# Kernel optimization log

Measured on AMD Instinct MI355X. Metric: run time of the kernel, lower is better.

Reference implementation:

```python
import jax, jax.numpy as jnp
import numpy as np

N = 20000          # num proposals (nodes)
E = 320000         # num edges
IN = 4096          # roi feature dim
EMB = 200          # glove embed dim
HID = 512          # hidden dim
NH = 8             # heads (conv1)
HC = HID // NH     # 64 per-head channels
NCLS = 151         # VG object classes
NEG_SLOPE = 0.2    # PyG GATConv leaky_relu slope


def setup_inputs() -> dict:
    key = jax.random.key(0)
    ks = jax.random.split(key, 18)
    d_in1 = IN + EMB + 128  # 4424, conv1 input dim
    inp = {
        "roi_features": jax.random.normal(ks[0], (N, IN), jnp.float32),
        "box_info": jax.random.uniform(ks[1], (N, 9), jnp.float32),
        # embedding tables
        "emb1": jax.random.normal(ks[2], (NCLS, EMB), jnp.float32) * 0.02,
        "emb2": jax.random.normal(ks[3], (NCLS, EMB), jnp.float32) * 0.02,
        # bbox MLP 9 -> 32 -> 128
        "bw1": jax.random.normal(ks[4], (9, 32), jnp.float32) / np.sqrt(9),
        "bb1": jnp.zeros((32,), jnp.float32),
        "bw2": jax.random.normal(ks[5], (32, 128), jnp.float32) / np.sqrt(32),
        "bb2": jnp.zeros((128,), jnp.float32),
        # GATConv1: d_in1 -> 8 heads x 64, concat
        "W1": jax.random.normal(ks[6], (d_in1, NH * HC), jnp.float32) / np.sqrt(d_in1),
        "a_src1": jax.random.normal(ks[7], (NH, HC), jnp.float32) * 0.1,
        "a_dst1": jax.random.normal(ks[8], (NH, HC), jnp.float32) * 0.1,
        "bias1": jnp.zeros((NH * HC,), jnp.float32),
        # GATConv2: 512 -> 512, 1 head, concat=False
        "W2": jax.random.normal(ks[9], (HID, HID), jnp.float32) / np.sqrt(HID),
        "a_src2": jax.random.normal(ks[10], (1, HID), jnp.float32) * 0.1,
        "a_dst2": jax.random.normal(ks[11], (1, HID), jnp.float32) * 0.1,
        "bias2": jnp.zeros((HID,), jnp.float32),
        # int inputs
        "obj_labels": jax.random.randint(ks[12], (N,), 0, NCLS, jnp.int32),
        "edge_index": jax.random.randint(ks[13], (2, E), 0, N, jnp.int32),
    }
    return inp


def _segment_softmax(logits, seg, n):
    # logits: [E, H]; softmax over edges sharing the same destination seg id
    m = jax.ops.segment_max(logits, seg, num_segments=n)
    e = jnp.exp(logits - m[seg])
    s = jax.ops.segment_sum(e, seg, num_segments=n)
    return e / (s[seg] + 1e-16)


def _gat_conv(x, src, dst, W, a_src, a_dst, bias, concat):
    # PyG GATConv (self-loops already included in src/dst); dropout off (eval)
    n = x.shape[0]
    H, C = a_src.shape
    h = (x @ W).reshape(n, H, C)                      # [N, H, C]
    al_s = jnp.einsum('nhc,hc->nh', h, a_src)         # [N, H]
    al_d = jnp.einsum('nhc,hc->nh', h, a_dst)
    logits = jax.nn.leaky_relu(al_s[src] + al_d[dst], NEG_SLOPE)  # [E, H]
    alpha = _segment_softmax(logits, dst, n)          # [E, H]
    out = jax.ops.segment_sum(alpha[:, :, None] * h[src], dst, num_segments=n)
    out = out.reshape(n, H * C) if concat else out.mean(axis=1)
    return out + bias


def reference(roi_features, box_info, emb1, emb2, bw1, bb1, bw2, bb2,
              W1, a_src1, a_dst1, bias1, W2, a_src2, a_dst2, bias2,
              obj_labels, edge_index):
    n = roi_features.shape[0]
    # predcls mode: GT labels -> embedding lookup
    obj_embed = emb1[obj_labels]                              # [N, 200]
    pos = jax.nn.relu(box_info @ bw1 + bb1)
    pos = jax.nn.relu(pos @ bw2 + bb2)                        # [N, 128]
    x = jnp.concatenate([roi_features, obj_embed, pos], -1)  # [N, 4424]

    # add self-loops (PyG GATConv default)
    ar = jnp.arange(n, dtype=edge_index.dtype)
    src = jnp.concatenate([edge_index[0], ar])
    dst = jnp.concatenate([edge_index[1], ar])

    edge_f1 = jax.nn.elu(_gat_conv(x, src, dst, W1, a_src1, a_dst1, bias1, True))
    obj_feats = _gat_conv(edge_f1, src, dst, W2, a_src2, a_dst2, bias2, False)

    obj_dists = jax.nn.one_hot(obj_labels, NCLS, dtype=jnp.float32)
    edge_pre_rep = jnp.concatenate([roi_features, obj_feats, emb2[obj_labels]], -1)
    return obj_dists, obj_labels, edge_pre_rep
```

## Files before the change

### kernel.cpp

```cpp
#include <hip/hip_runtime.h>
#include <hip/hip_bf16.h>

#define NNODES 20000
#define NEDGES 320000
#define ETOT   (NEDGES + NNODES)
#define KPADX  4224
#define MPAD   20096
#define NCLS   151
#define EPRW   4808
#define OUT_LAB_OFF  3020000L
#define OUT_EPR_OFF  3040000L
#define NSLOPE 0.2f

typedef __attribute__((ext_vector_type(8))) short bf16x8;
typedef __attribute__((ext_vector_type(4))) float f32x4;
typedef __attribute__((ext_vector_type(4))) short s16x4;

__device__ __forceinline__ short f2bf(float v) {
  union { __hip_bfloat16 b; short s; } u;
  u.b = __float2bfloat16(v);
  return u.s;
}

__device__ __forceinline__ float bf2f(short s) {
  union { float f; unsigned u; } x;
  x.u = ((unsigned)(unsigned short)s) << 16;
  return x.f;
}

__device__ __forceinline__ void gld16(const short* g, short* l) {
  __builtin_amdgcn_global_load_lds(
      (const __attribute__((address_space(1))) unsigned int*)g,
      (__attribute__((address_space(3))) unsigned int*)l, 16, 0, 0);
}

#define PB0 20000
#define PB1 (PB0 + 1584)
#define PB2 (PB1 + 2112)
#define PB3 (PB2 + 256)
#define PB4 (PB3 + 1329)
#define PB5 (PB4 + 151)

__global__ __launch_bounds__(256) void mega_prep_kernel(
    const float* __restrict__ roi, const float* __restrict__ box,
    const float* __restrict__ emb1, const float* __restrict__ emb2,
    const float* __restrict__ bw1, const float* __restrict__ bb1,
    const float* __restrict__ bw2, const float* __restrict__ bb2,
    const float* __restrict__ W1, const float* __restrict__ W2,
    const int* __restrict__ labels, const int* __restrict__ ei,
    short* __restrict__ x, short* __restrict__ w1t, short* __restrict__ w2t,
    short* __restrict__ ef1, int* __restrict__ deg,
    float* __restrict__ als1, float* __restrict__ ald1,
    float* __restrict__ als2, float* __restrict__ ald2,
    float* __restrict__ E1, float* __restrict__ dout) {
  const int b = blockIdx.x;
  const int tid = threadIdx.x;

  __shared__ float hid[32];
  __shared__ float bx[9];
  __shared__ float tile[32][33];

  if (b < PB0) {
    const int n = b;
    if (tid < 9) bx[tid] = box[n * 9 + tid];
    __syncthreads();
    if (tid < 32) {
      float a = bb1[tid];
#pragma unroll
      for (int i = 0; i < 9; ++i) a += bx[i] * bw1[i * 32 + tid];
      hid[tid] = a > 0.f ? a : 0.f;
    }
    __syncthreads();
    const long xrow = (long)n * KPADX;
    if (tid < 128) {
      float a = bb2[tid];
#pragma unroll
      for (int i = 0; i < 32; ++i) a += hid[i] * bw2[i * 128 + tid];
      a = a > 0.f ? a : 0.f;
      x[xrow + 4096 + tid] = f2bf(a);
    }
    const int lab = labels[n];
    float* epr = dout + OUT_EPR_OFF + (long)n * EPRW;
#pragma unroll
    for (int j = tid * 4; j < 4096; j += 1024) {
      const f32x4 v = *(const f32x4*)&roi[(long)n * 4096 + j];
      __builtin_nontemporal_store(v, (f32x4*)&epr[j]);
      s16x4 bb;
      bb.x = f2bf(v.x); bb.y = f2bf(v.y); bb.z = f2bf(v.z); bb.w = f2bf(v.w);
      *(s16x4*)&x[xrow + j] = bb;
    }
    if (tid < 50) {
      const int j = tid * 4;
      const f32x4 e2 = *(const f32x4*)&emb2[lab * 200 + j];
      __builtin_nontemporal_store(e2, (f32x4*)&epr[4608 + j]);
    }
    for (int j = tid; j < NCLS; j += 256)
      dout[(long)n * NCLS + j] = (j == lab) ? 1.f : 0.f;
    if (tid == 0) dout[OUT_LAB_OFF + n] = (float)lab;
  } else if (b < PB1) {
    const int t = (b - PB0) * 256 + tid;
    if (t < 96 * KPADX) x[(long)NNODES * KPADX + t] = 0;
    if (t < 96 * 512)   ef1[(long)NNODES * 512 + t] = 0;
    if (t < MPAD * 8)   { als1[t] = 0.f; ald1[t] = 0.f; }
    if (t < MPAD)       { als2[t] = 0.f; ald2[t] = 0.f; }
  } else if (b < PB2) {
    const int t = b - PB1;
    const int n0 = (t % 16) * 32;
    const int k0 = (t / 16) * 32;
    const int tx = tid & 31, ty = tid >> 5;
#pragma unroll
    for (int i = ty; i < 32; i += 8) {
      const int kp = k0 + i;
      const int src = kp < 4096 ? kp : kp + 200;
      tile[i][tx] = W1[(long)src * 512 + (n0 + tx)];
    }
    __syncthreads();
#pragma unroll
    for (int i = ty; i < 32; i += 8)
      w1t[(long)(n0 + i) * KPADX + (k0 + tx)] = f2bf(tile[tx][i]);
  } else if (b < PB3) {
    const int t = b - PB2;
    const int n0 = (t % 16) * 32;
    const int k0 = (t / 16) * 32;
    const int tx = tid & 31, ty = tid >> 5;
#pragma unroll
    for (int i = ty; i < 32; i += 8)
      tile[i][tx] = W2[(long)(k0 + i) * 512 + (n0 + tx)];
    __syncthreads();
#pragma unroll
    for (int i = ty; i < 32; i += 8)
      w2t[(long)(n0 + i) * 512 + (k0 + tx)] = f2bf(tile[tx][i]);
  } else if (b < PB4) {
    const int e = (b - PB3) * 256 + tid;
    if (e < ETOT) {
      const int d = (e < NEDGES) ? ei[NEDGES + e] : (e - NEDGES);
      atomicAdd(&deg[d], 1);
    }
  } else {
    const int c = b - PB4;
#pragma unroll
    for (int jj = 0; jj < 2; ++jj) {
      const int j = tid + jj * 256;
      float a = 0.f;
      for (int k = 0; k < 200; ++k)
        a += emb1[c * 200 + k] * W1[(long)(4096 + k) * 512 + j];
      E1[c * 512 + j] = a;
    }
  }
}

__global__ __launch_bounds__(256) void scan_kernel(const int* __restrict__ deg,
                                                   int* __restrict__ off,
                                                   int* __restrict__ cur) {
  __shared__ int part[256];
  const int tid = threadIdx.x;
  const int chunk = (NNODES + 255) / 256;
  int start = tid * chunk;
  int end = start + chunk; if (end > NNODES) end = NNODES;
  int s = 0;
  for (int i = start; i < end; ++i) s += deg[i];
  part[tid] = s;
  __syncthreads();
  for (int d = 1; d < 256; d <<= 1) {
    const int v = (tid >= d) ? part[tid - d] : 0;
    __syncthreads();
    part[tid] += v;
    __syncthreads();
  }
  int base = part[tid] - s;
  for (int i = start; i < end; ++i) { off[i] = base; cur[i] = base; base += deg[i]; }
}

__global__ void csr_fill_kernel(const int* __restrict__ ei, int* __restrict__ cur,
                                int* __restrict__ csrs) {
  const int e = blockIdx.x * 256 + threadIdx.x;
  if (e >= ETOT) return;
  const int s = (e < NEDGES) ? ei[e] : (e - NEDGES);
  const int d = (e < NEDGES) ? ei[NEDGES + e] : (e - NEDGES);
  unsigned slot = (unsigned)atomicAdd(&cur[d], 1);
  if (slot >= ETOT) slot = 0;
  csrs[slot] = s;
}

__global__ __launch_bounds__(256) void gemm_bt(const short* __restrict__ A,
                                               const short* __restrict__ BT,
                                               short* __restrict__ C,
                                               const float* __restrict__ aS,
                                               const float* __restrict__ aD,
                                               float* __restrict__ als,
                                               float* __restrict__ ald,
                                               const float* __restrict__ E1,
                                               const int* __restrict__ labels,
                                               int Kpad, int Ncols, int H) {
  __shared__ short As[4096];
  __shared__ short Bs[4096];
  const int tid = threadIdx.x;
  const int lane = tid & 63;
  const int w = tid >> 6;
  const int wr = w >> 1, wc = w & 1;
  const int nbn = Ncols >> 7;
  const long bm = (long)((int)blockIdx.x / nbn) * 128;
  const long bn = (long)((int)blockIdx.x % nbn) * 128;

  f32x4 acc[4][4] = {};

  const short* gA0 = A + (bm + w * 32 + (lane >> 2)) * (long)Kpad + (lane & 3) * 8;
  const short* gA1 = gA0 + 16L * Kpad;
  const short* gB0 = BT + (bn + w * 32 + (lane >> 2)) * (long)Kpad + (lane & 3) * 8;
  const short* gB1 = gB0 + 16L * Kpad;
  short* lA0 = &As[w * 1024];
  short* lA1 = &As[w * 1024 + 512];
  short* lB0 = &Bs[w * 1024];
  short* lB1 = &Bs[w * 1024 + 512];

  const int ar = (wr * 64 + (lane & 15)) * 32 + (lane >> 4) * 8;
  const int br = (wc * 64 + (lane & 15)) * 32 + (lane >> 4) * 8;

  for (int k0 = 0; k0 < Kpad; k0 += 32) {
    gld16(gA0, lA0); gld16(gA1, lA1);
    gld16(gB0, lB0); gld16(gB1, lB1);
    gA0 += 32; gA1 += 32; gB0 += 32; gB1 += 32;
    asm volatile("s_waitcnt vmcnt(0)" ::: "memory");
    __syncthreads();
    bf16x8 a[4], b[4];
#pragma unroll
    for (int mi = 0; mi < 4; ++mi) a[mi] = *(const bf16x8*)&As[ar + mi * 512];
#pragma unroll
    for (int ni = 0; ni < 4; ++ni) b[ni] = *(const bf16x8*)&Bs[br + ni * 512];
#pragma unroll
    for (int mi = 0; mi < 4; ++mi)
#pragma unroll
      for (int ni = 0; ni < 4; ++ni)
        acc[mi][ni] = __builtin_amdgcn_mfma_f32_16x16x32_bf16(a[mi], b[ni], acc[mi][ni], 0, 0, 0);
    __syncthreads();
  }

  const int colb = (int)bn + wc * 64 + (lane & 15);

  if (E1) {
#pragma unroll
    for (int mi = 0; mi < 4; ++mi) {
#pragma unroll
      for (int r = 0; r < 4; ++r) {
        const long row = bm + wr * 64 + mi * 16 + (lane >> 4) * 4 + r;
        const int lb = (row < NNODES) ? labels[row] : 0;
        const float* e1r = E1 + (long)lb * 512;
#pragma unroll
        for (int ni = 0; ni < 4; ++ni)
          acc[mi][ni][r] += e1r[colb + ni * 16];
      }
    }
  }

#pragma unroll
  for (int mi = 0; mi < 4; ++mi) {
#pragma unroll
    for (int ni = 0; ni < 4; ++ni) {
      const long row0 = bm + wr * 64 + mi * 16 + (lane >> 4) * 4;
      const long col  = bn + wc * 64 + ni * 16 + (lane & 15);
#pragma unroll
      for (int r = 0; r < 4; ++r)
        C[(row0 + r) * (long)Ncols + col] = f2bf(acc[mi][ni][r]);
    }
  }

  float asv[4], adv[4];
#pragma unroll
  for (int ni = 0; ni < 4; ++ni) {
    asv[ni] = aS[colb + ni * 16];
    adv[ni] = aD[colb + ni * 16];
  }
  const int head = (H == 8) ? (((int)bn >> 6) + wc) : 0;
#pragma unroll
  for (int mi = 0; mi < 4; ++mi) {
#pragma unroll
    for (int r = 0; r < 4; ++r) {
      float s = 0.f, d = 0.f;
#pragma unroll
      for (int ni = 0; ni < 4; ++ni) {
        const float v = acc[mi][ni][r];
        s += v * asv[ni];
        d += v * adv[ni];
      }
#pragma unroll
      for (int o = 1; o < 16; o <<= 1) {
        s += __shfl_xor(s, o);
        d += __shfl_xor(d, o);
      }
      if ((lane & 15) == 0) {
        const long row = bm + wr * 64 + mi * 16 + (lane >> 4) * 4 + r;
        atomicAdd(&als[row * H + head], s);
        atomicAdd(&ald[row * H + head], d);
      }
    }
  }
}

__global__ __launch_bounds__(256) void gather1_kernel(const int* __restrict__ off,
    const int* __restrict__ csrs,
    const float* __restrict__ als, const float* __restrict__ ald,
    const short* __restrict__ h1, const float* __restrict__ bias,
    short* __restrict__ ef1) {
  const int dn = blockIdx.x * 4 + (threadIdx.x >> 6);
  const int lane = threadIdx.x & 63;
  const int c0 = lane * 8;
  const int head = lane >> 3;
  const int beg = off[dn];
  const int end = (dn == NNODES - 1) ? ETOT : off[dn + 1];
  const float ad = ald[dn * 8 + head];
  float sum = 0.f;
  float acc[8] = {};
  for (int i = beg; i < end; ++i) {
    int s = csrs[i];
    if ((unsigned)s >= NNODES) s = 0;
    float l = als[s * 8 + head] + ad;
    l = l > 0.f ? l : NSLOPE * l;
    const float wgt = expf(l);
    sum += wgt;
    const bf16x8 hv = *(const bf16x8*)&h1[(long)s * 512 + c0];
#pragma unroll
    for (int j = 0; j < 8; ++j) acc[j] += wgt * bf2f(hv[j]);
  }
  const float inv = 1.f / (sum + 1e-16f);
  bf16x8 outv;
#pragma unroll
  for (int j = 0; j < 8; ++j) {
    float r = acc[j] * inv + bias[c0 + j];
    r = r > 0.f ? r : expm1f(r);
    outv[j] = f2bf(r);
  }
  *(bf16x8*)&ef1[(long)dn * 512 + c0] = outv;
}

__global__ __launch_bounds__(256) void gather2_kernel(const int* __restrict__ off,
    const int* __restrict__ csrs,
    const float* __restrict__ als, const float* __restrict__ ald,
    const short* __restrict__ h2, const float* __restrict__ bias,
    float* __restrict__ dout) {
  const int dn = blockIdx.x * 4 + (threadIdx.x >> 6);
  const int lane = threadIdx.x & 63;
  const int c0 = lane * 8;
  const int beg = off[dn];
  const int end = (dn == NNODES - 1) ? ETOT : off[dn + 1];
  const float ad = ald[dn];
  float sum = 0.f;
  float acc[8] = {};
  for (int i = beg; i < end; ++i) {
    int s = csrs[i];
    if ((unsigned)s >= NNODES) s = 0;
    float l = als[s] + ad;
    l = l > 0.f ? l : NSLOPE * l;
    const float wgt = expf(l);
    sum += wgt;
    const bf16x8 hv = *(const bf16x8*)&h2[(long)s * 512 + c0];
#pragma unroll
    for (int j = 0; j < 8; ++j) acc[j] += wgt * bf2f(hv[j]);
  }
  const float inv = 1.f / (sum + 1e-16f);
  float* epr = dout + OUT_EPR_OFF + (long)dn * EPRW + 4096;
  f32x4 o0, o1;
  o0.x = acc[0] * inv + bias[c0 + 0];
  o0.y = acc[1] * inv + bias[c0 + 1];
  o0.z = acc[2] * inv + bias[c0 + 2];
  o0.w = acc[3] * inv + bias[c0 + 3];
  o1.x = acc[4] * inv + bias[c0 + 4];
  o1.y = acc[5] * inv + bias[c0 + 5];
  o1.z = acc[6] * inv + bias[c0 + 6];
  o1.w = acc[7] * inv + bias[c0 + 7];
  __builtin_nontemporal_store(o0, (f32x4*)&epr[c0]);
  __builtin_nontemporal_store(o1, (f32x4*)&epr[c0 + 4]);
}

extern "C" void kernel_launch(void* const* d_in, const int* in_sizes, int n_in,
                              void* d_out, int out_size, void* d_ws, size_t ws_size,
                              hipStream_t stream) {
  const float* roi  = (const float*)d_in[0];
  const float* box  = (const float*)d_in[1];
  const float* emb1 = (const float*)d_in[2];
  const float* emb2 = (const float*)d_in[3];
  const float* bw1  = (const float*)d_in[4];
  const float* bb1  = (const float*)d_in[5];
  const float* bw2  = (const float*)d_in[6];
  const float* bb2  = (const float*)d_in[7];
  const float* W1   = (const float*)d_in[8];
  const float* as1  = (const float*)d_in[9];
  const float* ad1  = (const float*)d_in[10];
  const float* b1   = (const float*)d_in[11];
  const float* W2   = (const float*)d_in[12];
  const float* as2  = (const float*)d_in[13];
  const float* ad2  = (const float*)d_in[14];
  const float* b2   = (const float*)d_in[15];
  const int* labels = (const int*)d_in[16];
  const int* ei     = (const int*)d_in[17];
  float* dout = (float*)d_out;

  char* wsb = (char*)d_ws;
  size_t o = 0;
  auto alloc = [&](size_t bytes) -> void* {
    void* p = wsb + o;
    o += (bytes + 255) & ~(size_t)255;
    return p;
  };
  short* x    = (short*)alloc((size_t)MPAD * KPADX * 2);
  short* w1t  = (short*)alloc((size_t)512 * KPADX * 2);
  short* h1   = (short*)alloc((size_t)MPAD * 512 * 2);
  short* ef1  = (short*)alloc((size_t)MPAD * 512 * 2);
  short* w2t  = (short*)alloc((size_t)512 * 512 * 2);
  short* h2   = (short*)alloc((size_t)MPAD * 512 * 2);
  float* als1 = (float*)alloc((size_t)MPAD * 8 * 4);
  float* ald1 = (float*)alloc((size_t)MPAD * 8 * 4);
  float* als2 = (float*)alloc((size_t)MPAD * 4);
  float* ald2 = (float*)alloc((size_t)MPAD * 4);
  float* E1   = (float*)alloc((size_t)NCLS * 512 * 4);
  int*   deg  = (int*)alloc((size_t)NNODES * 4);
  int*   offs = (int*)alloc((size_t)NNODES * 4);
  int*   cur  = (int*)alloc((size_t)NNODES * 4);
  int*   csrs = (int*)alloc((size_t)ETOT * 4);

  const int EB = (ETOT + 255) / 256;

  hipMemsetAsync(deg, 0, (size_t)NNODES * 4, stream);

  hipLaunchKernelGGL(mega_prep_kernel, dim3(PB5), dim3(256), 0, stream,
                     roi, box, emb1, emb2, bw1, bb1, bw2, bb2, W1, W2,
                     labels, ei, x, w1t, w2t, ef1, deg,
                     als1, ald1, als2, ald2, E1, dout);
  hipLaunchKernelGGL(scan_kernel, dim3(1), dim3(256), 0, stream, deg, offs, cur);
  hipLaunchKernelGGL(csr_fill_kernel, dim3(EB), dim3(256), 0, stream, ei, cur, csrs);
  hipLaunchKernelGGL(gemm_bt, dim3(157 * 4), dim3(256), 0, stream,
                     x, w1t, h1, as1, ad1, als1, ald1, E1, labels,
                     KPADX, 512, 8);
  hipLaunchKernelGGL(gather1_kernel, dim3(NNODES / 4), dim3(256), 0, stream,
                     offs, csrs, als1, ald1, h1, b1, ef1);
  hipLaunchKernelGGL(gemm_bt, dim3(157 * 4), dim3(256), 0, stream,
                     ef1, w2t, h2, as2, ad2, als2, ald2,
                     (const float*)nullptr, (const int*)nullptr,
                     512, 512, 1);
  hipLaunchKernelGGL(gather2_kernel, dim3(NNODES / 4), dim3(256), 0, stream,
                     offs, csrs, als2, ald2, h2, b2, dout);
}
```

Baseline: 654.8 us.

## Split-K the conv1 GEMM and add a reduction kernel for bias and attention logits

The large conv1 projection GEMM (K=4224) is split four ways along K, so the grid grows from 628 to 2512 blocks and can fill more compute units. Each block writes bf16 partial sums to its own slice. A new reduce kernel adds the partials and the label-embedding term, writes h1, and computes the per-head attention source and destination logits. This costs an extra pass over four partial buffers and rounds each partial to bf16. The blocks are also reordered with an XCD-aware swizzle.

```diff
diff --git a/kernel.cpp b/kernel.cpp
--- a/kernel.cpp
+++ b/kernel.cpp
@@ -5,6 +5,8 @@
 #define NEDGES 320000
 #define ETOT   (NEDGES + NNODES)
 #define KPADX  4224
+#define SK     4
+#define KC     (KPADX / SK)
 #define MPAD   20096
 #define NCLS   151
 #define EPRW   4808
@@ -50,7 +52,6 @@
     const int* __restrict__ labels, const int* __restrict__ ei,
     short* __restrict__ x, short* __restrict__ w1t, short* __restrict__ w2t,
     short* __restrict__ ef1, int* __restrict__ deg,
-    float* __restrict__ als1, float* __restrict__ ald1,
     float* __restrict__ als2, float* __restrict__ ald2,
     float* __restrict__ E1, float* __restrict__ dout) {
   const int b = blockIdx.x;
@@ -101,7 +102,6 @@
     const int t = (b - PB0) * 256 + tid;
     if (t < 96 * KPADX) x[(long)NNODES * KPADX + t] = 0;
     if (t < 96 * 512)   ef1[(long)NNODES * 512 + t] = 0;
-    if (t < MPAD * 8)   { als1[t] = 0.f; ald1[t] = 0.f; }
     if (t < MPAD)       { als2[t] = 0.f; ald2[t] = 0.f; }
   } else if (b < PB2) {
     const int t = b - PB1;
@@ -182,6 +182,108 @@
   csrs[slot] = s;
 }
 
+__global__ __launch_bounds__(256) void gemm_split(const short* __restrict__ A,
+                                                  const short* __restrict__ BT,
+                                                  short* __restrict__ hp) {
+  __shared__ short As[4096];
+  __shared__ short Bs[4096];
+  const int tid = threadIdx.x;
+  const int lane = tid & 63;
+  const int w = tid >> 6;
+  const int wr = w >> 1, wc = w & 1;
+  const int wid = (blockIdx.x & 7) * 314 + ((int)blockIdx.x >> 3);
+  const long bm = (long)(wid >> 4) * 128;
+  const int  sk = (wid >> 2) & 3;
+  const long bn = (long)(wid & 3) * 128;
+
+  f32x4 acc[4][4] = {};
+
+  const short* gA0 = A + (bm + w * 32 + (lane >> 2)) * (long)KPADX + sk * KC + (lane & 3) * 8;
+  const short* gA1 = gA0 + 16L * KPADX;
+  const short* gB0 = BT + (bn + w * 32 + (lane >> 2)) * (long)KPADX + sk * KC + (lane & 3) * 8;
+  const short* gB1 = gB0 + 16L * KPADX;
+  short* lA0 = &As[w * 1024];
+  short* lA1 = &As[w * 1024 + 512];
+  short* lB0 = &Bs[w * 1024];
+  short* lB1 = &Bs[w * 1024 + 512];
+
+  const int ar = (wr * 64 + (lane & 15)) * 32 + (lane >> 4) * 8;
+  const int br = (wc * 64 + (lane & 15)) * 32 + (lane >> 4) * 8;
+
+  for (int k0 = 0; k0 < KC; k0 += 32) {
+    gld16(gA0, lA0); gld16(gA1, lA1);
+    gld16(gB0, lB0); gld16(gB1, lB1);
+    gA0 += 32; gA1 += 32; gB0 += 32; gB1 += 32;
+    asm volatile("s_waitcnt vmcnt(0)" ::: "memory");
+    __syncthreads();
+    bf16x8 a[4], b[4];
+#pragma unroll
+    for (int mi = 0; mi < 4; ++mi) a[mi] = *(const bf16x8*)&As[ar + mi * 512];
+#pragma unroll
+    for (int ni = 0; ni < 4; ++ni) b[ni] = *(const bf16x8*)&Bs[br + ni * 512];
+#pragma unroll
+    for (int mi = 0; mi < 4; ++mi)
+#pragma unroll
+      for (int ni = 0; ni < 4; ++ni)
+        acc[mi][ni] = __builtin_amdgcn_mfma_f32_16x16x32_bf16(a[mi], b[ni], acc[mi][ni], 0, 0, 0);
+    __syncthreads();
+  }
+
+  short* Cp = hp + (long)sk * MPAD * 512;
+#pragma unroll
+  for (int mi = 0; mi < 4; ++mi) {
+#pragma unroll
+    for (int ni = 0; ni < 4; ++ni) {
+      const long row0 = bm + wr * 64 + mi * 16 + (lane >> 4) * 4;
+      const long col  = bn + wc * 64 + ni * 16 + (lane & 15);
+#pragma unroll
+      for (int r = 0; r < 4; ++r)
+        Cp[(row0 + r) * 512 + col] = f2bf(acc[mi][ni][r]);
+    }
+  }
+}
+
+__global__ __launch_bounds__(256) void reduce1_kernel(short* __restrict__ hp,
+    const float* __restrict__ E1, const int* __restrict__ labels,
+    const float* __restrict__ aS, const float* __restrict__ aD,
+    float* __restrict__ als, float* __restrict__ ald) {
+  const int row = blockIdx.x * 4 + (threadIdx.x >> 6);
+  const int lane = threadIdx.x & 63;
+  const int c0 = lane * 8;
+  const long base = (long)row * 512 + c0;
+  float v[8] = {};
+#pragma unroll
+  for (int s = 0; s < SK; ++s) {
+    const bf16x8 p = *(const bf16x8*)&hp[(long)s * MPAD * 512 + base];
+#pragma unroll
+    for (int j = 0; j < 8; ++j) v[j] += bf2f(p[j]);
+  }
+  const int lab = (row < NNODES) ? labels[row] : 0;
+  const float* e1r = E1 + (long)lab * 512;
+#pragma unroll
+  for (int j = 0; j < 8; ++j) v[j] += e1r[c0 + j];
+  bf16x8 o;
+#pragma unroll
+  for (int j = 0; j < 8; ++j) o[j] = f2bf(v[j]);
+  *(bf16x8*)&hp[base] = o;
+  float s_ = 0.f, d_ = 0.f;
+#pragma unroll
+  for (int j = 0; j < 8; ++j) {
+    s_ += v[j] * aS[c0 + j];
+    d_ += v[j] * aD[c0 + j];
+  }
+#pragma unroll
+  for (int oo = 1; oo < 8; oo <<= 1) {
+    s_ += __shfl_xor(s_, oo);
+    d_ += __shfl_xor(d_, oo);
+  }
+  if ((lane & 7) == 0) {
+    const int head = lane >> 3;
+    als[row * 8 + head] = s_;
+    ald[row * 8 + head] = d_;
+  }
+}
+
 __global__ __launch_bounds__(256) void gemm_bt(const short* __restrict__ A,
                                                const short* __restrict__ BT,
                                                short* __restrict__ C,
@@ -189,8 +291,6 @@
                                                const float* __restrict__ aD,
                                                float* __restrict__ als,
                                                float* __restrict__ ald,
-                                               const float* __restrict__ E1,
-                                               const int* __restrict__ labels,
                                                int Kpad, int Ncols, int H) {
   __shared__ short As[4096];
   __shared__ short Bs[4096];
@@ -236,21 +336,6 @@
   }
 
   const int colb = (int)bn + wc * 64 + (lane & 15);
-
-  if (E1) {
-#pragma unroll
-    for (int mi = 0; mi < 4; ++mi) {
-#pragma unroll
-      for (int r = 0; r < 4; ++r) {
-        const long row = bm + wr * 64 + mi * 16 + (lane >> 4) * 4 + r;
-        const int lb = (row < NNODES) ? labels[row] : 0;
-        const float* e1r = E1 + (long)lb * 512;
-#pragma unroll
-        for (int ni = 0; ni < 4; ++ni)
-          acc[mi][ni][r] += e1r[colb + ni * 16];
-      }
-    }
-  }
 
 #pragma unroll
   for (int mi = 0; mi < 4; ++mi) {
@@ -403,7 +488,8 @@
   };
   short* x    = (short*)alloc((size_t)MPAD * KPADX * 2);
   short* w1t  = (short*)alloc((size_t)512 * KPADX * 2);
-  short* h1   = (short*)alloc((size_t)MPAD * 512 * 2);
+  short* hp   = (short*)alloc((size_t)SK * MPAD * 512 * 2);
+  short* h1   = hp;
   short* ef1  = (short*)alloc((size_t)MPAD * 512 * 2);
   short* w2t  = (short*)alloc((size_t)512 * 512 * 2);
   short* h2   = (short*)alloc((size_t)MPAD * 512 * 2);
@@ -424,18 +510,17 @@
   hipLaunchKernelGGL(mega_prep_kernel, dim3(PB5), dim3(256), 0, stream,
                      roi, box, emb1, emb2, bw1, bb1, bw2, bb2, W1, W2,
                      labels, ei, x, w1t, w2t, ef1, deg,
-                     als1, ald1, als2, ald2, E1, dout);
+                     als2, ald2, E1, dout);
   hipLaunchKernelGGL(scan_kernel, dim3(1), dim3(256), 0, stream, deg, offs, cur);
   hipLaunchKernelGGL(csr_fill_kernel, dim3(EB), dim3(256), 0, stream, ei, cur, csrs);
-  hipLaunchKernelGGL(gemm_bt, dim3(157 * 4), dim3(256), 0, stream,
-                     x, w1t, h1, as1, ad1, als1, ald1, E1, labels,
-                     KPADX, 512, 8);
+  hipLaunchKernelGGL(gemm_split, dim3(157 * SK * 4), dim3(256), 0, stream,
+                     x, w1t, hp);
+  hipLaunchKernelGGL(reduce1_kernel, dim3(MPAD / 4), dim3(256), 0, stream,
+                     hp, E1, labels, as1, ad1, als1, ald1);
   hipLaunchKernelGGL(gather1_kernel, dim3(NNODES / 4), dim3(256), 0, stream,
                      offs, csrs, als1, ald1, h1, b1, ef1);
   hipLaunchKernelGGL(gemm_bt, dim3(157 * 4), dim3(256), 0, stream,
-                     ef1, w2t, h2, as2, ad2, als2, ald2,
-                     (const float*)nullptr, (const int*)nullptr,
-                     512, 512, 1);
+                     ef1, w2t, h2, as2, ad2, als2, ald2, 512, 512, 1);
   hipLaunchKernelGGL(gather2_kernel, dim3(NNODES / 4), dim3(256), 0, stream,
                      offs, csrs, als2, ald2, h2, b2, dout);
 }
```

After: 565.1 us. 13.7% less time.
